# Kernel tuning notes

Measured on AMD Instinct MI355X. Metric: run time of the kernel, lower is better.

Reference implementation:

```python
import jax, jax.numpy as jnp
import numpy as np

BLOCK = 32          # MX block size (group_size)
E4M3_MAX = 448.0    # max finite value of float8_e4m3fn
E4M3_EMAX = 8       # max exponent of e4m3 (used for shared-exponent offset per MX spec)
TINY = 1e-38        # guard for log2(0)


def _quant_e4m3(v):
    """Fake-quantize v to the float8_e4m3fn grid with rint (round-half-even)."""
    a = jnp.abs(v)
    # exponent of each element, clamped to [min_normal_exp=-6, emax=8]
    e = jnp.clip(jnp.floor(jnp.log2(jnp.maximum(a, TINY))), -6.0, 8.0)
    step = jnp.exp2(e - 3.0)  # 3 mantissa bits
    q = jnp.clip(jnp.round(a / step) * step, 0.0, E4M3_MAX)
    return jnp.sign(v) * q


def mx_quant(v):
    """npu_dynamic_mx_quant(axis=-1, block_size=32, dst=e4m3, round=rint).
    Returns (q_blocks [..., K//32, 32], e8m0 scale [..., K//32])."""
    K = v.shape[-1]
    vb = v.reshape(*v.shape[:-1], K // BLOCK, BLOCK)
    amax = jnp.max(jnp.abs(vb), axis=-1)
    # shared exponent: floor(log2(amax)) - emax_elem, as an e8m0 power-of-two scale
    se = jnp.where(amax > 0,
                   jnp.floor(jnp.log2(jnp.maximum(amax, TINY))) - E4M3_EMAX,
                   0.0)
    scale = jnp.exp2(jnp.clip(se, -127.0, 127.0))
    q = _quant_e4m3(vb / scale[..., None])
    return q, scale


def setup_inputs() -> dict:
    key = jax.random.key(0)
    k1, k2, k3 = jax.random.split(key, 3)
    B, S, K, N = 2, 2048, 4096, 4096
    x = jax.random.normal(k1, (B, S, K), dtype=jnp.float32)
    weight = jax.random.normal(k2, (N, K), dtype=jnp.float32) * 0.02  # Linear weight [out, in]
    bias = jax.random.normal(k3, (N,), dtype=jnp.float32) * 0.01
    return {"x": x, "weight": weight, "bias": bias}


def reference(x, weight, bias):
    ori_shape = x.shape
    x2 = x.reshape(-1, ori_shape[-1])            # [M, K]
    # weight quantized once at init in the original module; same math here
    qw, sw = mx_quant(weight)                    # [N, K/32, 32], [N, K/32]
    qx, sx = mx_quant(x2)                        # [M, K/32, 32], [M, K/32]
    # group-scaled dequant-matmul: per-block scale product applied per group
    dqx = qx * sx[..., None]
    dqw = qw * sw[..., None]
    out = jnp.einsum('mgb,ngb->mn', dqx, dqw) + bias
    return out.reshape(*ori_shape[:-1], -1)
```

## Files before the change

kernel.cpp:

```cpp
#include <hip/hip_runtime.h>
#include <hip/hip_bf16.h>
#include <stdint.h>

typedef __attribute__((ext_vector_type(8)))  __bf16 bf16x8;
typedef __attribute__((ext_vector_type(16))) float  floatx16;
typedef unsigned short ushort8 __attribute__((ext_vector_type(8)));

__device__ __forceinline__ uint16_t f32_to_bf16_rn(float f) {
    uint32_t u = __float_as_uint(f);
    uint32_t r = u + 0x7FFFu + ((u >> 16) & 1u);
    return (uint16_t)(r >> 16);
}

__global__ __launch_bounds__(256) void quant_dq2_kernel(
    const float* __restrict__ x, const float* __restrict__ w,
    uint16_t* __restrict__ dqx, uint16_t* __restrict__ dqw,
    int nxh, int ntoth)
{
    int t = blockIdx.x * blockDim.x + threadIdx.x;
    if (t >= ntoth) return;
    const float* src; uint16_t* dst; int idx;
    if (t < nxh) { src = x; dst = dqx; idx = t; }
    else         { src = w; dst = dqw; idx = t - nxh; }

    const float4* p = (const float4*)src + (size_t)idx * 4;
    float4 v0 = p[0], v1 = p[1], v2 = p[2], v3 = p[3];
    float r[16] = {v0.x, v0.y, v0.z, v0.w, v1.x, v1.y, v1.z, v1.w,
                   v2.x, v2.y, v2.z, v2.w, v3.x, v3.y, v3.z, v3.w};

    float am = 0.0f;
#pragma unroll
    for (int i = 0; i < 16; ++i) am = fmaxf(am, fabsf(r[i]));
    am = fmaxf(am, __shfl_xor(am, 1));

    float scale, iscale;
    if (am > 0.0f) {
        int se = (int)((__float_as_uint(am) >> 23) & 0xFF) - 135;
        se = se < -127 ? -127 : se;
        scale  = __uint_as_float((uint32_t)(se + 127) << 23);
        iscale = __uint_as_float((uint32_t)(127 - se) << 23);
    } else {
        scale = 1.0f; iscale = 1.0f;
    }

    uint16_t o[16];
#pragma unroll
    for (int i = 0; i < 16; ++i) {
        float sv = r[i] * iscale;
        float a  = fabsf(sv);
        int e = (int)((__float_as_uint(a) >> 23) & 0xFF) - 127;
        e = e < -6 ? -6 : (e > 8 ? 8 : e);
        float step  = __uint_as_float((uint32_t)(e - 3 + 127) << 23);
        float rstep = __uint_as_float((uint32_t)(3 - e + 127) << 23);
        float q = rintf(a * rstep) * step;
        q = fminf(q, 448.0f);
        float dq = copysignf(q, sv) * scale;
        o[i] = f32_to_bf16_rn(dq);
    }
    ushort8 lo, hi;
#pragma unroll
    for (int i = 0; i < 8; ++i) { lo[i] = o[i]; hi[i] = o[i + 8]; }
    ((ushort8*)dst)[idx * 2]     = lo;
    ((ushort8*)dst)[idx * 2 + 1] = hi;
}

#define BM 256
#define BN 256
#define BK 64

__global__ __launch_bounds__(512, 2) void gemm_bt_bias(
    const uint16_t* __restrict__ A, const uint16_t* __restrict__ B,
    const float* __restrict__ bias, float* __restrict__ C,
    int M, int N, int K)
{
    extern __shared__ uint8_t lds[];
    uint16_t* sA = (uint16_t*)lds;
    uint16_t* sB = (uint16_t*)(lds + 65536);

    const int tid  = threadIdx.x;
    const int wave = tid >> 6;
    const int lane = tid & 63;

    int lin = blockIdx.y * gridDim.x + blockIdx.x;
    const int nwg = gridDim.x * gridDim.y;
    if ((nwg & 7) == 0) {
        const int q = nwg >> 3;
        lin = (lin & 7) * q + (lin >> 3);
    }
    const int bm = (lin / gridDim.x) * BM;
    const int bn = (lin % gridDim.x) * BN;

    const int srow   = tid >> 3;
    const int schunk = ((tid & 7) ^ (srow & 7)) * 8;
    const uint16_t* Ag = A + (size_t)(bm + srow) * K + schunk;
    const uint16_t* Bg = B + (size_t)(bn + srow) * K + schunk;
    const size_t c64K = (size_t)64 * K;
    uint8_t* dA0 = lds + wave * 1024;
    uint8_t* dB0 = lds + 65536 + wave * 1024;

    const int wm  = (wave >> 2) * 128;
    const int wn  = (wave & 3) * 64;
    const int m32 = lane & 31;
    const int h   = lane >> 5;
    const int swz = m32 & 7;

    floatx16 acc[4][2];
#pragma unroll
    for (int i = 0; i < 4; ++i)
#pragma unroll
        for (int j = 0; j < 2; ++j)
#pragma unroll
            for (int r = 0; r < 16; ++r) acc[i][j][r] = 0.0f;

    auto stage = [&](int buf, int tk) {
        const size_t k0 = (size_t)tk * BK;
        uint8_t* dA = dA0 + buf * 32768;
        uint8_t* dB = dB0 + buf * 32768;
#pragma unroll
        for (int c = 0; c < 4; ++c)
            __builtin_amdgcn_global_load_lds(
                (const __attribute__((address_space(1))) void*)(Ag + c * c64K + k0),
                (__attribute__((address_space(3))) void*)(dA + c * 8192), 16, 0, 0);
#pragma unroll
        for (int c = 0; c < 4; ++c)
            __builtin_amdgcn_global_load_lds(
                (const __attribute__((address_space(1))) void*)(Bg + c * c64K + k0),
                (__attribute__((address_space(3))) void*)(dB + c * 8192), 16, 0, 0);
    };

    const int NT = K / BK;
    stage(0, 0);

    for (int t = 0; t < NT; ++t) {
        const int cur = t & 1;
        if (t + 1 < NT) {
            stage(cur ^ 1, t + 1);
            asm volatile("s_waitcnt vmcnt(8)" ::: "memory");
        } else {
            asm volatile("s_waitcnt vmcnt(0)" ::: "memory");
        }
        __builtin_amdgcn_s_barrier();
        __builtin_amdgcn_sched_barrier(0);

        const uint16_t* bufA = sA + cur * 16384;
        const uint16_t* bufB = sB + cur * 16384;

        bf16x8 bB[2][4];
#pragma unroll
        for (int nj = 0; nj < 2; ++nj) {
            const int row = wn + nj * 32 + m32;
#pragma unroll
            for (int ks = 0; ks < 4; ++ks) {
                const int slot = (ks * 2 + h) ^ swz;
                bB[nj][ks] = *(const bf16x8*)(bufB + row * BK + slot * 8);
            }
        }
#pragma unroll
        for (int mi = 0; mi < 4; ++mi) {
            const int row = wm + mi * 32 + m32;
            bf16x8 aA[4];
#pragma unroll
            for (int ks = 0; ks < 4; ++ks) {
                const int slot = (ks * 2 + h) ^ swz;
                aA[ks] = *(const bf16x8*)(bufA + row * BK + slot * 8);
            }
            __builtin_amdgcn_s_setprio(1);
#pragma unroll
            for (int ks = 0; ks < 4; ++ks) {
                acc[mi][0] = __builtin_amdgcn_mfma_f32_32x32x16_bf16(aA[ks], bB[0][ks], acc[mi][0], 0, 0, 0);
                acc[mi][1] = __builtin_amdgcn_mfma_f32_32x32x16_bf16(aA[ks], bB[1][ks], acc[mi][1], 0, 0, 0);
            }
            __builtin_amdgcn_s_setprio(0);
        }
        __builtin_amdgcn_sched_barrier(0);
        __builtin_amdgcn_s_barrier();
    }

#pragma unroll
    for (int nj = 0; nj < 2; ++nj) {
        const int col = bn + wn + nj * 32 + m32;
        const float bz = bias[col];
#pragma unroll
        for (int mi = 0; mi < 4; ++mi) {
            const int rbase = bm + wm + mi * 32 + 4 * h;
#pragma unroll
            for (int r = 0; r < 16; ++r) {
                const int row = rbase + (r & 3) + 8 * (r >> 2);
                C[(size_t)row * N + col] = acc[mi][nj][r] + bz;
            }
        }
    }
}

extern "C" void kernel_launch(void* const* d_in, const int* in_sizes, int n_in,
                              void* d_out, int out_size, void* d_ws, size_t ws_size,
                              hipStream_t stream) {
    const float* x    = (const float*)d_in[0];
    const float* w    = (const float*)d_in[1];
    const float* bias = (const float*)d_in[2];
    float* out = (float*)d_out;

    const int N = in_sizes[2];
    const int K = in_sizes[1] / N;
    const int M = in_sizes[0] / K;

    uint16_t* dqx = (uint16_t*)d_ws;
    uint16_t* dqw = dqx + (size_t)M * K;

    const int nxh   = (M * K) / 16;
    const int ntoth = nxh + (N * K) / 16;
    quant_dq2_kernel<<<(ntoth + 255) / 256, 256, 0, stream>>>(x, w, dqx, dqw, nxh, ntoth);

    hipFuncSetAttribute((const void*)gemm_bt_bias,
                        hipFuncAttributeMaxDynamicSharedMemorySize, 131072);
    dim3 grid(N / BN, M / BM);
    gemm_bt_bias<<<grid, 512, 131072, stream>>>(dqx, dqw, bias, out, M, N, K);
}
```

Before: 291.5 us.

## Restructure GEMM into quadrant-staged 16x16x32 MFMA pipeline with split half-tile loads

```diff
diff --git a/kernel.cpp b/kernel.cpp
--- a/kernel.cpp
+++ b/kernel.cpp
@@ -3,7 +3,7 @@
 #include <stdint.h>
 
 typedef __attribute__((ext_vector_type(8)))  __bf16 bf16x8;
-typedef __attribute__((ext_vector_type(16))) float  floatx16;
+typedef __attribute__((ext_vector_type(4)))  float  floatx4;
 typedef unsigned short ushort8 __attribute__((ext_vector_type(8)));
 
 __device__ __forceinline__ uint16_t f32_to_bf16_rn(float f) {
@@ -68,14 +68,23 @@
 #define BN 256
 #define BK 64
 
+#define MM1(MH,NH,MI,NJ,KS,BF) \
+    acc[MH][NH][MI][NJ] = __builtin_amdgcn_mfma_f32_16x16x32_bf16( \
+        aF[MI][KS], BF[NJ][KS], acc[MH][NH][MI][NJ], 0, 0, 0)
+#define MMA_Q(MH,NH,BF) do { \
+    __builtin_amdgcn_s_setprio(1); \
+    MM1(MH,NH,0,0,0,BF); MM1(MH,NH,1,0,0,BF); MM1(MH,NH,2,0,0,BF); MM1(MH,NH,3,0,0,BF); \
+    MM1(MH,NH,0,1,0,BF); MM1(MH,NH,1,1,0,BF); MM1(MH,NH,2,1,0,BF); MM1(MH,NH,3,1,0,BF); \
+    MM1(MH,NH,0,0,1,BF); MM1(MH,NH,1,0,1,BF); MM1(MH,NH,2,0,1,BF); MM1(MH,NH,3,0,1,BF); \
+    MM1(MH,NH,0,1,1,BF); MM1(MH,NH,1,1,1,BF); MM1(MH,NH,2,1,1,BF); MM1(MH,NH,3,1,1,BF); \
+    __builtin_amdgcn_s_setprio(0); } while (0)
+
 __global__ __launch_bounds__(512, 2) void gemm_bt_bias(
     const uint16_t* __restrict__ A, const uint16_t* __restrict__ B,
     const float* __restrict__ bias, float* __restrict__ C,
     int M, int N, int K)
 {
     extern __shared__ uint8_t lds[];
-    uint16_t* sA = (uint16_t*)lds;
-    uint16_t* sB = (uint16_t*)(lds + 65536);
 
     const int tid  = threadIdx.x;
     const int wave = tid >> 6;
@@ -83,113 +92,137 @@
 
     int lin = blockIdx.y * gridDim.x + blockIdx.x;
     const int nwg = gridDim.x * gridDim.y;
-    if ((nwg & 7) == 0) {
-        const int q = nwg >> 3;
-        lin = (lin & 7) * q + (lin >> 3);
-    }
+    if ((nwg & 7) == 0) { const int q = nwg >> 3; lin = (lin & 7) * q + (lin >> 3); }
     const int bm = (lin / gridDim.x) * BM;
     const int bn = (lin % gridDim.x) * BN;
 
     const int srow   = tid >> 3;
-    const int schunk = ((tid & 7) ^ (srow & 7)) * 8;
-    const uint16_t* Ag = A + (size_t)(bm + srow) * K + schunk;
-    const uint16_t* Bg = B + (size_t)(bn + srow) * K + schunk;
-    const size_t c64K = (size_t)64 * K;
-    uint8_t* dA0 = lds + wave * 1024;
-    uint8_t* dB0 = lds + 65536 + wave * 1024;
-
-    const int wm  = (wave >> 2) * 128;
-    const int wn  = (wave & 3) * 64;
-    const int m32 = lane & 31;
-    const int h   = lane >> 5;
-    const int swz = m32 & 7;
-
-    floatx16 acc[4][2];
-#pragma unroll
-    for (int i = 0; i < 4; ++i)
-#pragma unroll
-        for (int j = 0; j < 2; ++j)
-#pragma unroll
-            for (int r = 0; r < 16; ++r) acc[i][j][r] = 0.0f;
-
-    auto stage = [&](int buf, int tk) {
-        const size_t k0 = (size_t)tk * BK;
-        uint8_t* dA = dA0 + buf * 32768;
-        uint8_t* dB = dB0 + buf * 32768;
-#pragma unroll
-        for (int c = 0; c < 4; ++c)
-            __builtin_amdgcn_global_load_lds(
-                (const __attribute__((address_space(1))) void*)(Ag + c * c64K + k0),
-                (__attribute__((address_space(3))) void*)(dA + c * 8192), 16, 0, 0);
-#pragma unroll
-        for (int c = 0; c < 4; ++c)
-            __builtin_amdgcn_global_load_lds(
-                (const __attribute__((address_space(1))) void*)(Bg + c * c64K + k0),
-                (__attribute__((address_space(3))) void*)(dB + c * 8192), 16, 0, 0);
+    const int schunk = (tid & 7) ^ (srow & 7);
+    const uint16_t* Asrc = A + (size_t)(bm + srow) * K + schunk * 8;
+    const uint16_t* Bsrc = B + (size_t)(bn + srow) * K + schunk * 8;
+    const size_t rowK = (size_t)64 * K;
+    const uint32_t dwave = wave * 1024;
+
+    auto stage = [&](int buf, int tk, int op, int h) {
+        const uint16_t* s = (op ? Bsrc : Asrc) + (size_t)tk * BK + (size_t)(2 * h) * rowK;
+        uint8_t* d = lds + buf * 65536 + op * 32768 + h * 16384 + dwave;
+        __builtin_amdgcn_global_load_lds(
+            (const __attribute__((address_space(1))) void*)(s),
+            (__attribute__((address_space(3))) void*)(d), 16, 0, 0);
+        __builtin_amdgcn_global_load_lds(
+            (const __attribute__((address_space(1))) void*)(s + rowK),
+            (__attribute__((address_space(3))) void*)(d + 8192), 16, 0, 0);
     };
 
+    const int g   = lane >> 4;
+    const int r16 = lane & 15;
+    const int swz = lane & 7;
+    const int w0m = (wave >> 2) * 64;
+    const int w0n = (wave & 3) * 32;
+
+    auto frag = [&](const uint8_t* panel, int row, int ks) -> bf16x8 {
+        const int slot = (ks * 4 + g) ^ swz;
+        return *(const bf16x8*)(panel + row * 128 + slot * 16);
+    };
+
+    floatx4 acc[2][2][4][2];
+#pragma unroll
+    for (int a0 = 0; a0 < 2; ++a0)
+#pragma unroll
+        for (int a1 = 0; a1 < 2; ++a1)
+#pragma unroll
+            for (int a2 = 0; a2 < 4; ++a2)
+#pragma unroll
+                for (int a3 = 0; a3 < 2; ++a3)
+#pragma unroll
+                    for (int a4 = 0; a4 < 4; ++a4) acc[a0][a1][a2][a3][a4] = 0.0f;
+
+    bf16x8 aF[4][2], bF0[2][2], bF1[2][2];
+
     const int NT = K / BK;
-    stage(0, 0);
+    stage(0, 0, 0, 0); stage(0, 0, 1, 0); stage(0, 0, 1, 1); stage(0, 0, 0, 1);
+    stage(1, 1, 0, 0); stage(1, 1, 1, 0); stage(1, 1, 1, 1);
+    asm volatile("s_waitcnt vmcnt(6)" ::: "memory");
+    __builtin_amdgcn_s_barrier();
 
     for (int t = 0; t < NT; ++t) {
-        const int cur = t & 1;
-        if (t + 1 < NT) {
-            stage(cur ^ 1, t + 1);
-            asm volatile("s_waitcnt vmcnt(8)" ::: "memory");
-        } else {
-            asm volatile("s_waitcnt vmcnt(0)" ::: "memory");
-        }
-        __builtin_amdgcn_s_barrier();
-        __builtin_amdgcn_sched_barrier(0);
-
-        const uint16_t* bufA = sA + cur * 16384;
-        const uint16_t* bufB = sB + cur * 16384;
-
-        bf16x8 bB[2][4];
+        const int cur = t & 1, nxt = cur ^ 1;
+        const uint8_t* bA = lds + cur * 65536;
+        const uint8_t* bB = bA + 32768;
+
+#pragma unroll
+        for (int mi = 0; mi < 4; ++mi) {
+            aF[mi][0] = frag(bA, w0m + mi * 16 + r16, 0);
+            aF[mi][1] = frag(bA, w0m + mi * 16 + r16, 1);
+        }
 #pragma unroll
         for (int nj = 0; nj < 2; ++nj) {
-            const int row = wn + nj * 32 + m32;
-#pragma unroll
-            for (int ks = 0; ks < 4; ++ks) {
-                const int slot = (ks * 2 + h) ^ swz;
-                bB[nj][ks] = *(const bf16x8*)(bufB + row * BK + slot * 8);
+            bF0[nj][0] = frag(bB, w0n + nj * 16 + r16, 0);
+            bF0[nj][1] = frag(bB, w0n + nj * 16 + r16, 1);
+        }
+        if (t + 1 < NT) stage(nxt, t + 1, 0, 1);
+        __builtin_amdgcn_sched_barrier(0);
+        __builtin_amdgcn_s_barrier();
+        asm volatile("s_waitcnt lgkmcnt(0)" ::: "memory");
+        __builtin_amdgcn_sched_barrier(0);
+        MMA_Q(0, 0, bF0);
+        __builtin_amdgcn_sched_barrier(0);
+        __builtin_amdgcn_s_barrier();
+
+#pragma unroll
+        for (int nj = 0; nj < 2; ++nj) {
+            bF1[nj][0] = frag(bB, w0n + 128 + nj * 16 + r16, 0);
+            bF1[nj][1] = frag(bB, w0n + 128 + nj * 16 + r16, 1);
+        }
+        if (t + 2 < NT) stage(cur, t + 2, 0, 0);
+        __builtin_amdgcn_sched_barrier(0);
+        __builtin_amdgcn_s_barrier();
+        asm volatile("s_waitcnt lgkmcnt(0)" ::: "memory");
+        __builtin_amdgcn_sched_barrier(0);
+        MMA_Q(0, 1, bF1);
+        __builtin_amdgcn_sched_barrier(0);
+        __builtin_amdgcn_s_barrier();
+
+#pragma unroll
+        for (int mi = 0; mi < 4; ++mi) {
+            aF[mi][0] = frag(bA, w0m + 128 + mi * 16 + r16, 0);
+            aF[mi][1] = frag(bA, w0m + 128 + mi * 16 + r16, 1);
+        }
+        if (t + 2 < NT) stage(cur, t + 2, 1, 0);
+        __builtin_amdgcn_sched_barrier(0);
+        __builtin_amdgcn_s_barrier();
+        asm volatile("s_waitcnt lgkmcnt(0)" ::: "memory");
+        __builtin_amdgcn_sched_barrier(0);
+        MMA_Q(1, 1, bF1);
+        __builtin_amdgcn_sched_barrier(0);
+        __builtin_amdgcn_s_barrier();
+
+        if (t + 2 < NT) stage(cur, t + 2, 1, 1);
+        __builtin_amdgcn_sched_barrier(0);
+        __builtin_amdgcn_s_barrier();
+        MMA_Q(1, 0, bF0);
+        __builtin_amdgcn_sched_barrier(0);
+        if (t < NT - 2) asm volatile("s_waitcnt vmcnt(6)" ::: "memory");
+        else            asm volatile("s_waitcnt vmcnt(0)" ::: "memory");
+        __builtin_amdgcn_s_barrier();
+    }
+
+#pragma unroll
+    for (int mh = 0; mh < 2; ++mh)
+#pragma unroll
+        for (int nh = 0; nh < 2; ++nh)
+#pragma unroll
+            for (int nj = 0; nj < 2; ++nj) {
+                const int col = bn + w0n + nh * 128 + nj * 16 + r16;
+                const float bz = bias[col];
+#pragma unroll
+                for (int mi = 0; mi < 4; ++mi) {
+                    const int rowb = bm + w0m + mh * 128 + mi * 16 + g * 4;
+#pragma unroll
+                    for (int rr = 0; rr < 4; ++rr)
+                        C[(size_t)(rowb + rr) * N + col] = acc[mh][nh][mi][nj][rr] + bz;
+                }
             }
-        }
-#pragma unroll
-        for (int mi = 0; mi < 4; ++mi) {
-            const int row = wm + mi * 32 + m32;
-            bf16x8 aA[4];
-#pragma unroll
-            for (int ks = 0; ks < 4; ++ks) {
-                const int slot = (ks * 2 + h) ^ swz;
-                aA[ks] = *(const bf16x8*)(bufA + row * BK + slot * 8);
-            }
-            __builtin_amdgcn_s_setprio(1);
-#pragma unroll
-            for (int ks = 0; ks < 4; ++ks) {
-                acc[mi][0] = __builtin_amdgcn_mfma_f32_32x32x16_bf16(aA[ks], bB[0][ks], acc[mi][0], 0, 0, 0);
-                acc[mi][1] = __builtin_amdgcn_mfma_f32_32x32x16_bf16(aA[ks], bB[1][ks], acc[mi][1], 0, 0, 0);
-            }
-            __builtin_amdgcn_s_setprio(0);
-        }
-        __builtin_amdgcn_sched_barrier(0);
-        __builtin_amdgcn_s_barrier();
-    }
-
-#pragma unroll
-    for (int nj = 0; nj < 2; ++nj) {
-        const int col = bn + wn + nj * 32 + m32;
-        const float bz = bias[col];
-#pragma unroll
-        for (int mi = 0; mi < 4; ++mi) {
-            const int rbase = bm + wm + mi * 32 + 4 * h;
-#pragma unroll
-            for (int r = 0; r < 16; ++r) {
-                const int row = rbase + (r & 3) + 8 * (r >> 2);
-                C[(size_t)row * N + col] = acc[mi][nj][r] + bz;
-            }
-        }
-    }
 }
 
 extern "C" void kernel_launch(void* const* d_in, const int* in_sizes, int n_in,
```

After: 273.2 us. 1.07x faster.
